# Optimization experiments

Hardware: AMD Instinct MI355X
Metric: run time of the kernel (lower is better)

## Reference

```python
import jax, jax.numpy as jnp
import numpy as np

NO_LAYERS = 2048
MODES = 4096
APL = 8          # action_per_layer
BATCH = 1        # forced to 1 by the final .view on a batch-1 tensor


def setup_inputs() -> dict:
    key = jax.random.key(0)
    ks = jax.random.split(key, 12)

    def cplx(k, shape):
        k1, k2 = jax.random.split(k)
        return (jax.random.uniform(k1, shape) + 1j * jax.random.uniform(k2, shape)).astype(jnp.complex64)

    return {
        "model_p": jax.random.normal(ks[0], (NO_LAYERS, MODES), dtype=jnp.float32),
        # complex spectral weights, torch.rand init on cfloat -> uniform real+imag
        "w_fft_0": cplx(ks[1], (1, MODES)),
        "w_fft_1": cplx(ks[2], (1, MODES)),
        "w_fft_2": cplx(ks[3], (1, MODES)),
        # lin1: no_layers -> modes
        "lin1_w": jax.random.normal(ks[4], (MODES, NO_LAYERS), dtype=jnp.float32) / np.sqrt(NO_LAYERS),
        "lin1_b": jnp.zeros((MODES,), dtype=jnp.float32),
        # lin2: modes -> no_layers * action_per_layer  (the big matvec, 268 MB)
        "lin2_w": jax.random.normal(ks[5], (NO_LAYERS * APL, MODES), dtype=jnp.float32) / np.sqrt(MODES),
        "lin2_b": jnp.zeros((NO_LAYERS * APL,), dtype=jnp.float32),
    }


def _space_time_fft_feature(data, w_fft):
    # data: (b, f, p) real or complex; w_fft: (1, modes) complex
    fft_data = jnp.fft.fft(data, norm='forward')                 # (b, f, p)
    # einsum contracts both p and n, leaving singleton m -> (b, f, 1)
    y = jnp.einsum('bfp,mn->bfm', fft_data, w_fft)
    iffw = jnp.fft.ifft(y, norm='forward')                       # (b, f, 1)
    return jnp.tanh(iffw).real                                   # complex tanh, take real


def reference(model_p, w_fft_0, w_fft_1, w_fft_2, lin1_w, lin1_b, lin2_w, lin2_b):
    x = _space_time_fft_feature(model_p[None], w_fft_0)          # (1, no_layers, 1)
    x = _space_time_fft_feature(x, w_fft_1)                      # (1, no_layers, 1)
    x = _space_time_fft_feature(x, w_fft_2)                      # (1, no_layers, 1)
    x = x.reshape(1, -1)                                         # (1, no_layers)
    x = jnp.tanh(x @ lin1_w.T + lin1_b)                          # (1, modes)
    x = (x @ lin2_w.T + lin2_b).reshape(BATCH, NO_LAYERS, APL)   # (1, no_layers, apl)
    return x
```

## Files before the change

kernel.cpp:

```cpp
#include <hip/hip_runtime.h>
#include <math.h>

#define NO_LAYERS 2048
#define MODES 4096
#define APL 8
#define OUT_N (NO_LAYERS * APL)

typedef float nf4 __attribute__((ext_vector_type(4)));

__device__ __forceinline__ float retanh_cplx(float t, float Sr, float Si) {
    float x = t * Sr;
    float y = t * Si;
    float a = 2.0f * fabsf(x);
    float e1 = expf(-a);
    float e2 = e1 * e1;
    float num = 1.0f - e2;
    float den = 1.0f + e2 + 2.0f * e1 * cosf(2.0f * y);
    return copysignf(num / den, x);
}

__global__ void __launch_bounds__(256) k_prep(const float* __restrict__ model_p,
                                              const float* __restrict__ w0,
                                              const float* __restrict__ w1,
                                              const float* __restrict__ w2,
                                              float* __restrict__ t_out) {
    __shared__ float red[3][2][4];
    __shared__ float S[3][2];
    const int tid = threadIdx.x;
    const int wave = tid >> 6, lane = tid & 63;

    const float* wptr[3] = {w0, w1, w2};
    float sr[3] = {0.f, 0.f, 0.f}, si[3] = {0.f, 0.f, 0.f};
    #pragma unroll
    for (int w = 0; w < 3; w++) {
        const float2* p = (const float2*)wptr[w];
        for (int i = tid; i < MODES; i += 256) {
            float2 v = p[i];
            sr[w] += v.x; si[w] += v.y;
        }
    }
    #pragma unroll
    for (int off = 32; off > 0; off >>= 1) {
        #pragma unroll
        for (int w = 0; w < 3; w++) {
            sr[w] += __shfl_down(sr[w], off);
            si[w] += __shfl_down(si[w], off);
        }
    }
    if (lane == 0) {
        #pragma unroll
        for (int w = 0; w < 3; w++) { red[w][0][wave] = sr[w]; red[w][1][wave] = si[w]; }
    }
    __syncthreads();
    if (tid == 0) {
        #pragma unroll
        for (int w = 0; w < 3; w++) {
            S[w][0] = red[w][0][0] + red[w][0][1] + red[w][0][2] + red[w][0][3];
            S[w][1] = red[w][1][0] + red[w][1][1] + red[w][1][2] + red[w][1][3];
        }
    }
    __syncthreads();
    const float S0r = S[0][0], S0i = S[0][1];
    const float S1r = S[1][0], S1i = S[1][1];
    const float S2r = S[2][0], S2i = S[2][1];

    const int f = blockIdx.x * 256 + tid;
    float t = model_p[(size_t)f * MODES];
    t = retanh_cplx(t, S0r, S0i);
    t = retanh_cplx(t, S1r, S1i);
    t = retanh_cplx(t, S2r, S2i);
    t_out[f] = t;
}

__global__ void __launch_bounds__(256) k_lin1(const float* __restrict__ t,
                                              const float* __restrict__ w,
                                              const float* __restrict__ b,
                                              float* __restrict__ h) {
    __shared__ float ts[NO_LAYERS];
    const int tid = threadIdx.x;
    {
        const float4* tp = (const float4*)t;
        float4* sp = (float4*)ts;
        for (int i = tid; i < NO_LAYERS / 4; i += 256) sp[i] = tp[i];
    }
    __syncthreads();
    const int wave = tid >> 6, lane = tid & 63;
    const int row = blockIdx.x * 4 + wave;
    const nf4* wp = (const nf4*)(w + (size_t)row * NO_LAYERS);
    const float4* tp = (const float4*)ts;
    float acc = 0.f;
    #pragma unroll
    for (int i = 0; i < (NO_LAYERS / 4) / 64; i++) {
        int idx = i * 64 + lane;
        nf4 wv = __builtin_nontemporal_load(&wp[idx]);
        float4 tv = tp[idx];
        acc += wv.x * tv.x + wv.y * tv.y + wv.z * tv.z + wv.w * tv.w;
    }
    #pragma unroll
    for (int off = 32; off > 0; off >>= 1) acc += __shfl_down(acc, off);
    if (lane == 0) h[row] = tanhf(acc + b[row]);
}

__global__ void __launch_bounds__(256) k_lin2(const float* __restrict__ h,
                                              const float* __restrict__ w,
                                              const float* __restrict__ b,
                                              float* __restrict__ out) {
    __shared__ float hs[MODES];
    const int tid = threadIdx.x;
    {
        const float4* hp = (const float4*)h;
        float4* sp = (float4*)hs;
        for (int i = tid; i < MODES / 4; i += 256) sp[i] = hp[i];
    }
    __syncthreads();
    const int wave = tid >> 6, lane = tid & 63;
    const int row0 = blockIdx.x * 8 + wave * 2;
    const nf4* wp0 = (const nf4*)(w + (size_t)row0 * MODES);
    const nf4* wp1 = (const nf4*)(w + (size_t)(row0 + 1) * MODES);
    const float4* hp = (const float4*)hs;
    float acc0 = 0.f, acc1 = 0.f;
    #pragma unroll
    for (int i = 0; i < (MODES / 4) / 64; i++) {
        int idx = i * 64 + lane;
        float4 hv = hp[idx];
        nf4 w0v = __builtin_nontemporal_load(&wp0[idx]);
        nf4 w1v = __builtin_nontemporal_load(&wp1[idx]);
        acc0 += w0v.x * hv.x + w0v.y * hv.y + w0v.z * hv.z + w0v.w * hv.w;
        acc1 += w1v.x * hv.x + w1v.y * hv.y + w1v.z * hv.z + w1v.w * hv.w;
    }
    #pragma unroll
    for (int off = 32; off > 0; off >>= 1) {
        acc0 += __shfl_down(acc0, off);
        acc1 += __shfl_down(acc1, off);
    }
    if (lane == 0) {
        out[row0]     = acc0 + b[row0];
        out[row0 + 1] = acc1 + b[row0 + 1];
    }
}

extern "C" void kernel_launch(void* const* d_in, const int* in_sizes, int n_in,
                              void* d_out, int out_size, void* d_ws, size_t ws_size,
                              hipStream_t stream) {
    const float* model_p = (const float*)d_in[0];
    const float* w0      = (const float*)d_in[1];
    const float* w1      = (const float*)d_in[2];
    const float* w2      = (const float*)d_in[3];
    const float* lin1_w  = (const float*)d_in[4];
    const float* lin1_b  = (const float*)d_in[5];
    const float* lin2_w  = (const float*)d_in[6];
    const float* lin2_b  = (const float*)d_in[7];
    float* out = (float*)d_out;

    float* t = (float*)d_ws;
    float* h = t + NO_LAYERS;

    k_prep<<<8, 256, 0, stream>>>(model_p, w0, w1, w2, t);
    k_lin1<<<1024, 256, 0, stream>>>(t, lin1_w, lin1_b, h);
    k_lin2<<<2048, 256, 0, stream>>>(h, lin2_w, lin2_b, out);
}
```

Measured before the change: 390.7 us.

## Fuse FFT-feature prep into lin1 and prefetch weights before shared-memory staging

The prep kernel, which reduces the spectral weights and applies three complex tanh stages, is folded into the lin1 kernel. Each of the 1024 blocks now recomputes the weight sums and all 2048 tanh features itself. This removes one launch and the round trip through global memory, at the price of redundant work per block. lin1 and lin2 now issue their first weight-row loads before staging the input vector into shared memory and waiting on the barrier, so that memory latency overlaps the staging.

```diff
diff --git a/kernel.cpp b/kernel.cpp
--- a/kernel.cpp
+++ b/kernel.cpp
@@ -19,82 +19,76 @@
     return copysignf(num / den, x);
 }
 
-__global__ void __launch_bounds__(256) k_prep(const float* __restrict__ model_p,
-                                              const float* __restrict__ w0,
-                                              const float* __restrict__ w1,
-                                              const float* __restrict__ w2,
-                                              float* __restrict__ t_out) {
+__global__ void __launch_bounds__(256) k_lin1f(const float* __restrict__ model_p,
+                                               const float* __restrict__ w0,
+                                               const float* __restrict__ w1,
+                                               const float* __restrict__ w2,
+                                               const float* __restrict__ w,
+                                               const float* __restrict__ b,
+                                               float* __restrict__ h) {
     __shared__ float red[3][2][4];
     __shared__ float S[3][2];
+    __shared__ float ts[NO_LAYERS];
     const int tid = threadIdx.x;
     const int wave = tid >> 6, lane = tid & 63;
+
+    const int row = blockIdx.x * 4 + wave;
+    const nf4* wp = (const nf4*)(w + (size_t)row * NO_LAYERS);
+    nf4 wv[(NO_LAYERS / 4) / 64];
+    #pragma unroll
+    for (int i = 0; i < (NO_LAYERS / 4) / 64; i++)
+        wv[i] = __builtin_nontemporal_load(&wp[i * 64 + lane]);
 
     const float* wptr[3] = {w0, w1, w2};
     float sr[3] = {0.f, 0.f, 0.f}, si[3] = {0.f, 0.f, 0.f};
     #pragma unroll
-    for (int w = 0; w < 3; w++) {
-        const float2* p = (const float2*)wptr[w];
-        for (int i = tid; i < MODES; i += 256) {
-            float2 v = p[i];
-            sr[w] += v.x; si[w] += v.y;
+    for (int q = 0; q < 3; q++) {
+        const float2* p = (const float2*)wptr[q];
+        #pragma unroll
+        for (int i = 0; i < MODES / 256; i++) {
+            float2 v = p[i * 256 + tid];
+            sr[q] += v.x; si[q] += v.y;
         }
     }
     #pragma unroll
     for (int off = 32; off > 0; off >>= 1) {
         #pragma unroll
-        for (int w = 0; w < 3; w++) {
-            sr[w] += __shfl_down(sr[w], off);
-            si[w] += __shfl_down(si[w], off);
+        for (int q = 0; q < 3; q++) {
+            sr[q] += __shfl_down(sr[q], off);
+            si[q] += __shfl_down(si[q], off);
         }
     }
     if (lane == 0) {
         #pragma unroll
-        for (int w = 0; w < 3; w++) { red[w][0][wave] = sr[w]; red[w][1][wave] = si[w]; }
+        for (int q = 0; q < 3; q++) { red[q][0][wave] = sr[q]; red[q][1][wave] = si[q]; }
     }
     __syncthreads();
-    if (tid == 0) {
-        #pragma unroll
-        for (int w = 0; w < 3; w++) {
-            S[w][0] = red[w][0][0] + red[w][0][1] + red[w][0][2] + red[w][0][3];
-            S[w][1] = red[w][1][0] + red[w][1][1] + red[w][1][2] + red[w][1][3];
-        }
+    if (tid < 6) {
+        int q = tid >> 1, c = tid & 1;
+        S[q][c] = red[q][c][0] + red[q][c][1] + red[q][c][2] + red[q][c][3];
     }
     __syncthreads();
     const float S0r = S[0][0], S0i = S[0][1];
     const float S1r = S[1][0], S1i = S[1][1];
     const float S2r = S[2][0], S2i = S[2][1];
 
-    const int f = blockIdx.x * 256 + tid;
-    float t = model_p[(size_t)f * MODES];
-    t = retanh_cplx(t, S0r, S0i);
-    t = retanh_cplx(t, S1r, S1i);
-    t = retanh_cplx(t, S2r, S2i);
-    t_out[f] = t;
-}
-
-__global__ void __launch_bounds__(256) k_lin1(const float* __restrict__ t,
-                                              const float* __restrict__ w,
-                                              const float* __restrict__ b,
-                                              float* __restrict__ h) {
-    __shared__ float ts[NO_LAYERS];
-    const int tid = threadIdx.x;
-    {
-        const float4* tp = (const float4*)t;
-        float4* sp = (float4*)ts;
-        for (int i = tid; i < NO_LAYERS / 4; i += 256) sp[i] = tp[i];
+    #pragma unroll
+    for (int k = 0; k < NO_LAYERS / 256; k++) {
+        const int f = k * 256 + tid;
+        float t = model_p[(size_t)f * MODES];
+        t = retanh_cplx(t, S0r, S0i);
+        t = retanh_cplx(t, S1r, S1i);
+        t = retanh_cplx(t, S2r, S2i);
+        ts[f] = t;
     }
     __syncthreads();
-    const int wave = tid >> 6, lane = tid & 63;
-    const int row = blockIdx.x * 4 + wave;
-    const nf4* wp = (const nf4*)(w + (size_t)row * NO_LAYERS);
+
     const float4* tp = (const float4*)ts;
     float acc = 0.f;
     #pragma unroll
     for (int i = 0; i < (NO_LAYERS / 4) / 64; i++) {
-        int idx = i * 64 + lane;
-        nf4 wv = __builtin_nontemporal_load(&wp[idx]);
-        float4 tv = tp[idx];
-        acc += wv.x * tv.x + wv.y * tv.y + wv.z * tv.z + wv.w * tv.w;
+        float4 tv = tp[i * 64 + lane];
+        acc += wv[i].x * tv.x + wv[i].y * tv.y + wv[i].z * tv.z + wv[i].w * tv.w;
     }
     #pragma unroll
     for (int off = 32; off > 0; off >>= 1) acc += __shfl_down(acc, off);
@@ -107,21 +101,37 @@
                                               float* __restrict__ out) {
     __shared__ float hs[MODES];
     const int tid = threadIdx.x;
-    {
-        const float4* hp = (const float4*)h;
-        float4* sp = (float4*)hs;
-        for (int i = tid; i < MODES / 4; i += 256) sp[i] = hp[i];
-    }
-    __syncthreads();
     const int wave = tid >> 6, lane = tid & 63;
     const int row0 = blockIdx.x * 8 + wave * 2;
     const nf4* wp0 = (const nf4*)(w + (size_t)row0 * MODES);
     const nf4* wp1 = (const nf4*)(w + (size_t)(row0 + 1) * MODES);
+
+    nf4 pw0[4], pw1[4];
+    #pragma unroll
+    for (int i = 0; i < 4; i++) {
+        pw0[i] = __builtin_nontemporal_load(&wp0[i * 64 + lane]);
+        pw1[i] = __builtin_nontemporal_load(&wp1[i * 64 + lane]);
+    }
+
+    {
+        const float4* hp = (const float4*)h;
+        float4* sp = (float4*)hs;
+        #pragma unroll
+        for (int i = 0; i < (MODES / 4) / 256; i++) sp[i * 256 + tid] = hp[i * 256 + tid];
+    }
+    __syncthreads();
+
     const float4* hp = (const float4*)hs;
     float acc0 = 0.f, acc1 = 0.f;
     #pragma unroll
-    for (int i = 0; i < (MODES / 4) / 64; i++) {
-        int idx = i * 64 + lane;
+    for (int i = 0; i < 4; i++) {
+        float4 hv = hp[i * 64 + lane];
+        acc0 += pw0[i].x * hv.x + pw0[i].y * hv.y + pw0[i].z * hv.z + pw0[i].w * hv.w;
+        acc1 += pw1[i].x * hv.x + pw1[i].y * hv.y + pw1[i].z * hv.z + pw1[i].w * hv.w;
+    }
+    #pragma unroll
+    for (int i = 4; i < (MODES / 4) / 64; i++) {
+        const int idx = i * 64 + lane;
         float4 hv = hp[idx];
         nf4 w0v = __builtin_nontemporal_load(&wp0[idx]);
         nf4 w1v = __builtin_nontemporal_load(&wp1[idx]);
@@ -152,10 +162,8 @@
     const float* lin2_b  = (const float*)d_in[7];
     float* out = (float*)d_out;
 
-    float* t = (float*)d_ws;
-    float* h = t + NO_LAYERS;
+    float* h = (float*)d_ws;
 
-    k_prep<<<8, 256, 0, stream>>>(model_p, w0, w1, w2, t);
-    k_lin1<<<1024, 256, 0, stream>>>(t, lin1_w, lin1_b, h);
+    k_lin1f<<<1024, 256, 0, stream>>>(model_p, w0, w1, w2, lin1_w, lin1_b, h);
     k_lin2<<<2048, 256, 0, stream>>>(h, lin2_w, lin2_b, out);
 }
```

Measured after the change: 387.4 us. About the same (-0.9%).
